# Kernel optimization log

Hardware: AMD Instinct MI355X
Metric: run time of the kernel (lower is better)

## Reference

```python
import jax, jax.numpy as jnp
import numpy as np

EMB = 256
HEADS = 8
D_HEAD = EMB // HEADS


def apply_rope(x):
    # x: [B, H, T, D] (interleaved-pair RoPE, matching the torch source)
    T, D = x.shape[-2], x.shape[-1]
    freqs = 10000.0 ** (-jnp.arange(0, D, 2, dtype=jnp.float32) / D)  # [D/2]
    angles = jnp.arange(T, dtype=jnp.float32)[:, None] * freqs[None, :]  # [T, D/2]
    sin = jnp.repeat(jnp.sin(angles), 2, axis=1)  # [T, D]
    cos = jnp.repeat(jnp.cos(angles), 2, axis=1)  # [T, D]
    x1 = x[..., 0::2]
    x2 = x[..., 1::2]
    rotated = jnp.stack((-x2, x1), axis=-1).reshape(x.shape)  # interleave (-x2, x1)
    return x * cos + rotated * sin


def setup_inputs() -> dict:
    key = jax.random.key(0)
    k1, k2, k3, k4, k5 = jax.random.split(key, 5)
    B, T = 8, 2048
    x = jax.random.normal(k1, (B, T, EMB), dtype=jnp.float32)
    s = 1.0 / np.sqrt(EMB)
    # Linear weights stored as [in, out] (torch weight.T), y = x @ W + b
    Wqkv = jax.random.uniform(k2, (EMB, 3 * EMB), minval=-s, maxval=s, dtype=jnp.float32)
    bqkv = jax.random.uniform(k3, (3 * EMB,), minval=-s, maxval=s, dtype=jnp.float32)
    Wout = jax.random.uniform(k4, (EMB, EMB), minval=-s, maxval=s, dtype=jnp.float32)
    bout = jax.random.uniform(k5, (EMB,), minval=-s, maxval=s, dtype=jnp.float32)
    return {"x": x, "Wqkv": Wqkv, "bqkv": bqkv, "Wout": Wout, "bout": bout}


def reference(x, Wqkv, bqkv, Wout, bout):
    B, T, E = x.shape
    H, Dh = HEADS, D_HEAD
    qkv = x @ Wqkv + bqkv  # [B, T, 3E]
    qkv = qkv.reshape(B, T, 3, H, Dh).transpose(2, 0, 3, 1, 4)  # [3, B, H, T, Dh]
    q, k, v = qkv[0], qkv[1], qkv[2]
    q = apply_rope(q)
    k = apply_rope(k)
    scores = jnp.einsum('bhtd,bhsd->bhts', q, k) / np.sqrt(Dh)  # [B, H, T, T]
    causal = jnp.triu(jnp.ones((T, T), dtype=bool), k=1)
    scores = jnp.where(causal, -jnp.inf, scores)
    attn = jax.nn.softmax(scores, axis=-1)
    out = jnp.einsum('bhts,bhsd->bthd', attn, v).reshape(B, T, E)
    return out @ Wout + bout
```

## Files before the change

### kernel.cpp

```cpp
#include <hip/hip_runtime.h>
#include <hip/hip_bf16.h>
#include <math.h>

typedef __hip_bfloat16 bf16;
using s8v = __attribute__((ext_vector_type(8))) short;
using f4v = __attribute__((ext_vector_type(4))) float;

__device__ __forceinline__ float bfb2f(unsigned short u) {
    return __uint_as_float(((unsigned int)u) << 16);
}
__device__ __forceinline__ unsigned short f2bfb(float f) {
    unsigned int u = __float_as_uint(f);
    unsigned int r = (u + 0x7fffu + ((u >> 16) & 1u)) >> 16;
    return (unsigned short)r;
}
__device__ __forceinline__ unsigned int packbf2(float a, float b) {
    return __builtin_amdgcn_perm(__float_as_uint(b) + 0x8000u,
                                 __float_as_uint(a) + 0x8000u,
                                 0x07060302u);
}

__device__ __forceinline__ void gload_lds16(const void* g, void* l) {
    __builtin_amdgcn_global_load_lds(
        (const __attribute__((address_space(1))) unsigned int*)g,
        (__attribute__((address_space(3))) unsigned int*)l, 16, 0, 0);
}

__device__ __forceinline__ int sniff_fp32(const void* p, int tid, int* s_flag)
{
    if (tid == 0) *s_flag = 0;
    __syncthreads();
    const uint4* u = (const uint4*)p;
    int local = 0;
    #pragma unroll
    for (int i = 0; i < 4; i++) {
        const uint4 v = u[i * 256 + tid];
        if ((v.x & 0x7F80u) == 0x7F80u) local = 1;
        if ((v.y & 0x7F80u) == 0x7F80u) local = 1;
        if ((v.z & 0x7F80u) == 0x7F80u) local = 1;
        if ((v.w & 0x7F80u) == 0x7F80u) local = 1;
    }
    if (local) atomicOr(s_flag, 1);
    __syncthreads();
    return *s_flag;
}

__global__ __launch_bounds__(256)
void k_prep(const void* __restrict__ x, const void* __restrict__ Wqkv,
            const void* __restrict__ bqkv, const void* __restrict__ Wout,
            const void* __restrict__ bout,
            bf16* __restrict__ wqkvT, bf16* __restrict__ woutT,
            float* __restrict__ bq_f, float* __restrict__ bo_f,
            bf16* __restrict__ xb)
{
    __shared__ int sf;
    const int bid = blockIdx.x;
    const int tid = threadIdx.x;
    if (bid < 768) {
        const int f = sniff_fp32(Wqkv, tid, &sf);
        unsigned short v = f ? f2bfb(((const float*)Wqkv)[(size_t)tid * 768 + bid])
                             : ((const unsigned short*)Wqkv)[(size_t)tid * 768 + bid];
        ((unsigned short*)wqkvT)[(size_t)bid * 256 + tid] = v;
        if (bid < 12) {
            const int i = bid * 256 + tid;
            bq_f[i] = f ? ((const float*)bqkv)[i]
                        : bfb2f(((const unsigned short*)bqkv)[i]);
        }
    } else if (bid < 1024) {
        const int n = bid - 768;
        const int f = sniff_fp32(Wout, tid, &sf);
        unsigned short v = f ? f2bfb(((const float*)Wout)[(size_t)tid * 256 + n])
                             : ((const unsigned short*)Wout)[(size_t)tid * 256 + n];
        ((unsigned short*)woutT)[(size_t)n * 256 + tid] = v;
        if (n == 0)
            bo_f[tid] = f ? ((const float*)bout)[tid]
                          : bfb2f(((const unsigned short*)bout)[tid]);
    } else {
        const int f = sniff_fp32(x, tid, &sf);
        if (f) {
            const size_t cb = (size_t)(bid - 1024) * 4096;
            #pragma unroll
            for (int i = 0; i < 4; i++) {
                const size_t e = cb + (size_t)i * 1024 + tid * 4;
                const float4 v = *(const float4*)((const float*)x + e);
                ushort4 o4;
                o4.x = f2bfb(v.x);
                o4.y = f2bfb(v.y);
                o4.z = f2bfb(v.z);
                o4.w = f2bfb(v.w);
                *(ushort4*)((unsigned short*)xb + e) = o4;
            }
        } else {
            const size_t base = (size_t)(bid - 1024) * 4096 + (size_t)tid * 16;
            const uint4* xu = (const uint4*)((const unsigned short*)x + base);
            uint4* dp = (uint4*)((unsigned short*)xb + base);
            dp[0] = xu[0];
            dp[1] = xu[1];
        }
    }
}

__global__ __launch_bounds__(256)
void k_qkv_rope(const bf16* __restrict__ xb, const bf16* __restrict__ wqkvT,
                const float* __restrict__ bq_f,
                bf16* __restrict__ q_ws, bf16* __restrict__ k_ws,
                bf16* __restrict__ vT_ws)
{
    __shared__ __align__(16) unsigned short Bls[4][8][512];
    __shared__ __align__(16) unsigned short Tls[4][1536];

    const int tid = threadIdx.x;
    const int bx = blockIdx.x;
    const int by = blockIdx.y;
    const int n0 = bx * 64;

    const int w    = tid >> 6;
    const int lane = tid & 63;
    const int col  = lane & 15;
    const int quad = lane >> 4;
    const int which = n0 >> 8;
    const int b     = (by * 128) >> 11;
    unsigned short* Tw = Tls[w];

    #pragma unroll
    for (int kk = 0; kk < 8; kk++)
        gload_lds16((const unsigned short*)wqkvT +
                        (size_t)(n0 + w * 16 + col) * 256 + kk * 32 + quad * 8,
                    &Bls[w][kk][0]);
    __syncthreads();

    for (int mi = 0; mi < 2; mi++) {
        const int T0 = by * 128 + mi * 64 + w * 16;

        f4v acc[4] = {{0.f,0.f,0.f,0.f}, {0.f,0.f,0.f,0.f},
                      {0.f,0.f,0.f,0.f}, {0.f,0.f,0.f,0.f}};

        #pragma unroll
        for (int kk = 0; kk < 8; kk++) {
            const s8v av = *(const s8v*)((const unsigned short*)xb +
                           (size_t)(T0 + col) * 256 + kk * 32 + quad * 8);
            #pragma unroll
            for (int c = 0; c < 4; c++) {
                const s8v bv = *(const s8v*)&Bls[c][kk][lane * 8];
                acc[c] = __builtin_amdgcn_mfma_f32_16x16x32_bf16(av, bv, acc[c], 0, 0, 0);
            }
        }

        const int t_base = ((by * 128) & 2047) + mi * 64 + w * 16;

        if (which == 2) {
            #pragma unroll
            for (int c = 0; c < 4; c++) {
                const int nl = c * 16 + col;
                const float bias = bq_f[n0 + nl];
                #pragma unroll
                for (int r = 0; r < 4; r++)
                    Tw[nl * 24 + quad * 4 + r] = f2bfb(acc[c][r] + bias);
            }
            const int ng = n0 + lane;
            const int h = (ng & 255) >> 5;
            const int d = ng & 31;
            const s8v t0 = *(const s8v*)&Tw[lane * 24];
            const s8v t1 = *(const s8v*)&Tw[lane * 24 + 8];
            unsigned short* dp = (unsigned short*)vT_ws +
                ((size_t)(b * 8 + h) * 32 + d) * 2048 + t_base;
            *(s8v*)dp = t0;
            *(s8v*)(dp + 8) = t1;
        } else {
            #pragma unroll
            for (int c = 0; c < 4; c++) {
                const int nl = c * 16 + col;
                const int d = (n0 + nl) & 31;
                const float bias = bq_f[n0 + nl];
                const float frev = __expf(-0.28782314f * (float)(d & ~1))
                                 * 0.15915494309189535f;
                #pragma unroll
                for (int r = 0; r < 4; r++) {
                    const float v = acc[c][r] + bias;
                    const float vp = __shfl_xor(v, 1);
                    const int t = t_base + quad * 4 + r;
                    float rev = (float)t * frev;
                    rev -= floorf(rev);
                    const float ang = rev * 6.283185307179586f;
                    const float sn = __sinf(ang);
                    const float cs = __cosf(ang);
                    float o = (d & 1) ? (v * cs + vp * sn)
                                      : (v * cs - vp * sn);
                    if (which == 0) o *= 0.17677669529663687f;
                    Tw[(quad * 4 + r) * 80 + nl] = f2bfb(o);
                }
            }
            const int row = lane >> 2;
            const int ch  = lane & 3;
            const int ng  = n0 + ch * 16;
            const int h   = (ng & 255) >> 5;
            const int d   = ng & 31;
            const int t   = t_base + row;
            const s8v t0 = *(const s8v*)&Tw[row * 80 + ch * 16];
            const s8v t1 = *(const s8v*)&Tw[row * 80 + ch * 16 + 8];
            unsigned short* dp = (unsigned short*)(which ? k_ws : q_ws) +
                ((size_t)(b * 8 + h) * 2048 + t) * 32 + d;
            *(s8v*)dp = t0;
            *(s8v*)(dp + 8) = t1;
        }
    }
}

__global__ __launch_bounds__(256, 4)
void k_attn(const bf16* __restrict__ q_ws, const bf16* __restrict__ k_ws,
            const bf16* __restrict__ vT_ws, bf16* __restrict__ ctx)
{
    __shared__ __align__(16) unsigned short KVls[2][8][512];
    __shared__ __align__(16) unsigned short Pls[4][16 * 72];

    const int tid  = threadIdx.x;
    const int w    = tid >> 6;
    const int lane = tid & 63;
    const int col  = lane & 15;
    const int quad = lane >> 4;

    const int idx = blockIdx.x;
    const int g   = idx >> 3;
    const int bhh = g >> 4;
    const int bx  = (g + bhh) & 15;
    const int bh  = (bhh << 3) | (idx & 7);
    const int mbA = bx;
    const int mbB = 31 - bx;
    const int T0a = mbA * 64 + w * 16;
    const int T0b = mbB * 64 + w * 16;

    const bf16* qb = q_ws  + (size_t)bh * 65536;
    const bf16* kb = k_ws  + (size_t)bh * 65536;
    const bf16* vb = vT_ws + (size_t)bh * 65536;

    const bf16* kg = kb + (size_t)(w * 16 + col) * 32 + quad * 8;
    const bf16* vg = vb + (size_t)(col + (w & 1) * 16) * 2048
                        + (w >> 1) * 32 + quad * 8;

    const s8v qaA = *(const s8v*)(qb + (size_t)(T0a + col) * 32 + quad * 8);
    const s8v qaB = *(const s8v*)(qb + (size_t)(T0b + col) * 32 + quad * 8);

    f4v oA0 = {0.f,0.f,0.f,0.f}, oA1 = {0.f,0.f,0.f,0.f};
    f4v oB0 = {0.f,0.f,0.f,0.f}, oB1 = {0.f,0.f,0.f,0.f};
    float lpA[4] = {0.f,0.f,0.f,0.f};
    float lpB[4] = {0.f,0.f,0.f,0.f};

    unsigned short* Pw = Pls[w];

    gload_lds16(kg, &KVls[0][w][0]);
    gload_lds16(vg, &KVls[0][4 + w][0]);
    __syncthreads();

    int cur = 0;
    for (int kblk = 0; kblk <= mbB; kblk++) {
        const int s0 = kblk * 64;
        const bool actA = (kblk <= mbA);

        if (kblk < mbB) {
            gload_lds16(kg + (size_t)(kblk + 1) * 2048, &KVls[cur ^ 1][w][0]);
            gload_lds16(vg + (kblk + 1) * 64,           &KVls[cur ^ 1][4 + w][0]);
        }

        const s8v kf0 = *(const s8v*)&KVls[cur][0][lane * 8];
        const s8v kf1 = *(const s8v*)&KVls[cur][1][lane * 8];
        const s8v kf2 = *(const s8v*)&KVls[cur][2][lane * 8];
        const s8v kf3 = *(const s8v*)&KVls[cur][3][lane * 8];
        const s8v v00 = *(const s8v*)&KVls[cur][4][lane * 8];
        const s8v v10 = *(const s8v*)&KVls[cur][5][lane * 8];
        const s8v v01 = *(const s8v*)&KVls[cur][6][lane * 8];
        const s8v v11 = *(const s8v*)&KVls[cur][7][lane * 8];

        const f4v z = {0.f, 0.f, 0.f, 0.f};
        f4v sB[4], sA[4];
        sB[0] = __builtin_amdgcn_mfma_f32_16x16x32_bf16(kf0, qaB, z, 0, 0, 0);
        sB[1] = __builtin_amdgcn_mfma_f32_16x16x32_bf16(kf1, qaB, z, 0, 0, 0);
        sB[2] = __builtin_amdgcn_mfma_f32_16x16x32_bf16(kf2, qaB, z, 0, 0, 0);
        sB[3] = __builtin_amdgcn_mfma_f32_16x16x32_bf16(kf3, qaB, z, 0, 0, 0);
        if (actA) {
            sA[0] = __builtin_amdgcn_mfma_f32_16x16x32_bf16(kf0, qaA, z, 0, 0, 0);
            sA[1] = __builtin_amdgcn_mfma_f32_16x16x32_bf16(kf1, qaA, z, 0, 0, 0);
            sA[2] = __builtin_amdgcn_mfma_f32_16x16x32_bf16(kf2, qaA, z, 0, 0, 0);
            sA[3] = __builtin_amdgcn_mfma_f32_16x16x32_bf16(kf3, qaA, z, 0, 0, 0);
        }

        if (kblk == mbB) {
            #pragma unroll
            for (int c = 0; c < 4; c++) {
                const int sbase = s0 + c * 16 + quad * 4;
                #pragma unroll
                for (int r = 0; r < 4; r++)
                    if (sbase + r > T0b + col) sB[c][r] = -INFINITY;
            }
        }
        if (actA && kblk == mbA) {
            #pragma unroll
            for (int c = 0; c < 4; c++) {
                const int sbase = s0 + c * 16 + quad * 4;
                #pragma unroll
                for (int r = 0; r < 4; r++)
                    if (sbase + r > T0a + col) sA[c][r] = -INFINITY;
            }
        }

        #pragma unroll
        for (int c = 0; c < 4; c++) {
            const float p0 = __expf(sB[c][0]);
            const float p1 = __expf(sB[c][1]);
            const float p2 = __expf(sB[c][2]);
            const float p3 = __expf(sB[c][3]);
            lpB[0] += p0; lpB[1] += p1; lpB[2] += p2; lpB[3] += p3;
            uint2 ww;
            ww.x = packbf2(p0, p1);
            ww.y = packbf2(p2, p3);
            *(uint2*)(Pw + col * 72 + c * 16 + quad * 4) = ww;
        }
        {
            const s8v pb0 = *(const s8v*)&Pw[col * 72 + quad * 8];
            const s8v pb1 = *(const s8v*)&Pw[col * 72 + 32 + quad * 8];
            oB0 = __builtin_amdgcn_mfma_f32_16x16x32_bf16(pb0, v00, oB0, 0, 0, 0);
            oB1 = __builtin_amdgcn_mfma_f32_16x16x32_bf16(pb0, v10, oB1, 0, 0, 0);
            oB0 = __builtin_amdgcn_mfma_f32_16x16x32_bf16(pb1, v01, oB0, 0, 0, 0);
            oB1 = __builtin_amdgcn_mfma_f32_16x16x32_bf16(pb1, v11, oB1, 0, 0, 0);
        }

        if (actA) {
            #pragma unroll
            for (int c = 0; c < 4; c++) {
                const float p0 = __expf(sA[c][0]);
                const float p1 = __expf(sA[c][1]);
                const float p2 = __expf(sA[c][2]);
                const float p3 = __expf(sA[c][3]);
                lpA[0] += p0; lpA[1] += p1; lpA[2] += p2; lpA[3] += p3;
                uint2 ww;
                ww.x = packbf2(p0, p1);
                ww.y = packbf2(p2, p3);
                *(uint2*)(Pw + col * 72 + c * 16 + quad * 4) = ww;
            }
            const s8v pa0 = *(const s8v*)&Pw[col * 72 + quad * 8];
            const s8v pa1 = *(const s8v*)&Pw[col * 72 + 32 + quad * 8];
            oA0 = __builtin_amdgcn_mfma_f32_16x16x32_bf16(pa0, v00, oA0, 0, 0, 0);
            oA1 = __builtin_amdgcn_mfma_f32_16x16x32_bf16(pa0, v10, oA1, 0, 0, 0);
            oA0 = __builtin_amdgcn_mfma_f32_16x16x32_bf16(pa1, v01, oA0, 0, 0, 0);
            oA1 = __builtin_amdgcn_mfma_f32_16x16x32_bf16(pa1, v11, oA1, 0, 0, 0);
        }

        __syncthreads();
        cur ^= 1;
    }

    float rsA = lpA[0] + lpA[1] + lpA[2] + lpA[3];
    rsA += __shfl_xor(rsA, 16);
    rsA += __shfl_xor(rsA, 32);
    float rsB = lpB[0] + lpB[1] + lpB[2] + lpB[3];
    rsB += __shfl_xor(rsB, 16);
    rsB += __shfl_xor(rsB, 32);

    const int b = bh >> 3;
    const int h = bh & 7;
    unsigned short* cp = (unsigned short*)ctx;
    #pragma unroll
    for (int tt = 0; tt < 2; tt++) {
        const int T0 = tt ? T0b : T0a;
        const float rs = tt ? rsB : rsA;
        #pragma unroll
        for (int r = 0; r < 4; r++) {
            const float inv = 1.0f / __shfl(rs, quad * 4 + r);
            const float e0 = (tt ? oB0[r] : oA0[r]) * inv;
            const float e1 = (tt ? oB1[r] : oA1[r]) * inv;
            const int t = T0 + quad * 4 + r;
            unsigned short* dst = cp + (size_t)(b * 2048 + t) * 256 + h * 32;
            dst[col]      = f2bfb(e0);
            dst[col + 16] = f2bfb(e1);
        }
    }
}

__global__ __launch_bounds__(256)
void k_outproj(const bf16* __restrict__ ctx, const bf16* __restrict__ woutT,
               const float* __restrict__ bo_f, float* __restrict__ out)
{
    __shared__ __align__(16) unsigned short Bls[4][8][512];

    const int tid = threadIdx.x;
    const int bx = blockIdx.x;
    const int by = blockIdx.y;
    const int n0 = bx * 64;

    const int w    = tid >> 6;
    const int lane = tid & 63;
    const int col  = lane & 15;
    const int quad = lane >> 4;

    #pragma unroll
    for (int kk = 0; kk < 8; kk++)
        gload_lds16((const unsigned short*)woutT +
                        (size_t)(n0 + w * 16 + col) * 256 + kk * 32 + quad * 8,
                    &Bls[w][kk][0]);
    __syncthreads();

    for (int mi = 0; mi < 2; mi++) {
        const int T0 = by * 128 + mi * 64 + w * 16;

        f4v acc[4] = {{0.f,0.f,0.f,0.f}, {0.f,0.f,0.f,0.f},
                      {0.f,0.f,0.f,0.f}, {0.f,0.f,0.f,0.f}};

        #pragma unroll
        for (int kk = 0; kk < 8; kk++) {
            const s8v av = *(const s8v*)((const unsigned short*)ctx +
                                         (size_t)(T0 + col) * 256 + kk * 32 + quad * 8);
            #pragma unroll
            for (int c = 0; c < 4; c++) {
                const s8v bv = *(const s8v*)&Bls[c][kk][lane * 8];
                acc[c] = __builtin_amdgcn_mfma_f32_16x16x32_bf16(av, bv, acc[c], 0, 0, 0);
            }
        }

        #pragma unroll
        for (int c = 0; c < 4; c++) {
            const int n = n0 + c * 16 + col;
            const float bias = bo_f[n];
            #pragma unroll
            for (int r = 0; r < 4; r++)
                out[(size_t)(T0 + quad * 4 + r) * 256 + n] = acc[c][r] + bias;
        }
    }
}

extern "C" void kernel_launch(void* const* d_in, const int* in_sizes, int n_in,
                              void* d_out, int out_size, void* d_ws, size_t ws_size,
                              hipStream_t stream)
{
    const void* x    = d_in[0];
    const void* Wqkv = d_in[1];
    const void* bqkv = d_in[2];
    const void* Wout = d_in[3];
    const void* bout = d_in[4];
    float* out = (float*)d_out;

    const size_t NQ = (size_t)8 * 8 * 2048 * 32;
    bf16* q_ws   = (bf16*)d_ws;
    bf16* k_ws   = q_ws + NQ;
    bf16* vT_ws  = k_ws + NQ;
    bf16* ctx    = vT_ws + NQ;
    bf16* xb     = ctx;
    bf16* wqkvT  = ctx + NQ;
    bf16* woutT  = wqkvT + (size_t)768 * 256;
    float* bq_f  = (float*)(woutT + (size_t)256 * 256);
    float* bo_f  = bq_f + 3072;

    k_prep    <<<2048,          256, 0, stream>>>(x, Wqkv, bqkv, Wout, bout,
                                                  wqkvT, woutT, bq_f, bo_f, xb);
    k_qkv_rope<<<dim3(12, 128), 256, 0, stream>>>(xb, wqkvT, bq_f,
                                                  q_ws, k_ws, vT_ws);
    k_attn    <<<1024,          256, 0, stream>>>(q_ws, k_ws, vT_ws, ctx);
    k_outproj <<<dim3(4, 128),  256, 0, stream>>>(ctx, woutT, bo_f, out);
}
```

Measured before the change: 158.8 us.

## Replace paired causal query blocks with one query block per attention workgroup

```diff
diff --git a/kernel.cpp b/kernel.cpp
--- a/kernel.cpp
+++ b/kernel.cpp
@@ -220,14 +220,9 @@
     const int quad = lane >> 4;
 
     const int idx = blockIdx.x;
-    const int g   = idx >> 3;
-    const int bhh = g >> 4;
-    const int bx  = (g + bhh) & 15;
-    const int bh  = (bhh << 3) | (idx & 7);
-    const int mbA = bx;
-    const int mbB = 31 - bx;
-    const int T0a = mbA * 64 + w * 16;
-    const int T0b = mbB * 64 + w * 16;
+    const int bh  = idx & 63;
+    const int mb  = 31 - (idx >> 6);
+    const int T0  = mb * 64 + w * 16;
 
     const bf16* qb = q_ws  + (size_t)bh * 65536;
     const bf16* kb = k_ws  + (size_t)bh * 65536;
@@ -237,13 +232,10 @@
     const bf16* vg = vb + (size_t)(col + (w & 1) * 16) * 2048
                         + (w >> 1) * 32 + quad * 8;
 
-    const s8v qaA = *(const s8v*)(qb + (size_t)(T0a + col) * 32 + quad * 8);
-    const s8v qaB = *(const s8v*)(qb + (size_t)(T0b + col) * 32 + quad * 8);
-
-    f4v oA0 = {0.f,0.f,0.f,0.f}, oA1 = {0.f,0.f,0.f,0.f};
-    f4v oB0 = {0.f,0.f,0.f,0.f}, oB1 = {0.f,0.f,0.f,0.f};
-    float lpA[4] = {0.f,0.f,0.f,0.f};
-    float lpB[4] = {0.f,0.f,0.f,0.f};
+    const s8v qa = *(const s8v*)(qb + (size_t)(T0 + col) * 32 + quad * 8);
+
+    f4v o0 = {0.f,0.f,0.f,0.f}, o1 = {0.f,0.f,0.f,0.f};
+    float lp[4] = {0.f,0.f,0.f,0.f};
 
     unsigned short* Pw = Pls[w];
 
@@ -252,13 +244,12 @@
     __syncthreads();
 
     int cur = 0;
-    for (int kblk = 0; kblk <= mbB; kblk++) {
-        const int s0 = kblk * 64;
-        const bool actA = (kblk <= mbA);
-
-        if (kblk < mbB) {
-            gload_lds16(kg + (size_t)(kblk + 1) * 2048, &KVls[cur ^ 1][w][0]);
-            gload_lds16(vg + (kblk + 1) * 64,           &KVls[cur ^ 1][4 + w][0]);
+    for (int kt = 0; kt <= mb; kt++) {
+        const int s0 = kt * 64;
+
+        if (kt < mb) {
+            gload_lds16(kg + (size_t)(kt + 1) * 2048, &KVls[cur ^ 1][w][0]);
+            gload_lds16(vg + (kt + 1) * 64,           &KVls[cur ^ 1][4 + w][0]);
         }
 
         const s8v kf0 = *(const s8v*)&KVls[cur][0][lane * 8];
@@ -271,107 +262,64 @@
         const s8v v11 = *(const s8v*)&KVls[cur][7][lane * 8];
 
         const f4v z = {0.f, 0.f, 0.f, 0.f};
-        f4v sB[4], sA[4];
-        sB[0] = __builtin_amdgcn_mfma_f32_16x16x32_bf16(kf0, qaB, z, 0, 0, 0);
-        sB[1] = __builtin_amdgcn_mfma_f32_16x16x32_bf16(kf1, qaB, z, 0, 0, 0);
-        sB[2] = __builtin_amdgcn_mfma_f32_16x16x32_bf16(kf2, qaB, z, 0, 0, 0);
-        sB[3] = __builtin_amdgcn_mfma_f32_16x16x32_bf16(kf3, qaB, z, 0, 0, 0);
-        if (actA) {
-            sA[0] = __builtin_amdgcn_mfma_f32_16x16x32_bf16(kf0, qaA, z, 0, 0, 0);
-            sA[1] = __builtin_amdgcn_mfma_f32_16x16x32_bf16(kf1, qaA, z, 0, 0, 0);
-            sA[2] = __builtin_amdgcn_mfma_f32_16x16x32_bf16(kf2, qaA, z, 0, 0, 0);
-            sA[3] = __builtin_amdgcn_mfma_f32_16x16x32_bf16(kf3, qaA, z, 0, 0, 0);
-        }
-
-        if (kblk == mbB) {
+        f4v s[4];
+        s[0] = __builtin_amdgcn_mfma_f32_16x16x32_bf16(kf0, qa, z, 0, 0, 0);
+        s[1] = __builtin_amdgcn_mfma_f32_16x16x32_bf16(kf1, qa, z, 0, 0, 0);
+        s[2] = __builtin_amdgcn_mfma_f32_16x16x32_bf16(kf2, qa, z, 0, 0, 0);
+        s[3] = __builtin_amdgcn_mfma_f32_16x16x32_bf16(kf3, qa, z, 0, 0, 0);
+
+        if (kt == mb) {
             #pragma unroll
             for (int c = 0; c < 4; c++) {
                 const int sbase = s0 + c * 16 + quad * 4;
                 #pragma unroll
                 for (int r = 0; r < 4; r++)
-                    if (sbase + r > T0b + col) sB[c][r] = -INFINITY;
-            }
-        }
-        if (actA && kblk == mbA) {
-            #pragma unroll
-            for (int c = 0; c < 4; c++) {
-                const int sbase = s0 + c * 16 + quad * 4;
-                #pragma unroll
-                for (int r = 0; r < 4; r++)
-                    if (sbase + r > T0a + col) sA[c][r] = -INFINITY;
+                    if (sbase + r > T0 + col) s[c][r] = -INFINITY;
             }
         }
 
         #pragma unroll
         for (int c = 0; c < 4; c++) {
-            const float p0 = __expf(sB[c][0]);
-            const float p1 = __expf(sB[c][1]);
-            const float p2 = __expf(sB[c][2]);
-            const float p3 = __expf(sB[c][3]);
-            lpB[0] += p0; lpB[1] += p1; lpB[2] += p2; lpB[3] += p3;
+            const float p0 = __expf(s[c][0]);
+            const float p1 = __expf(s[c][1]);
+            const float p2 = __expf(s[c][2]);
+            const float p3 = __expf(s[c][3]);
+            lp[0] += p0; lp[1] += p1; lp[2] += p2; lp[3] += p3;
             uint2 ww;
             ww.x = packbf2(p0, p1);
             ww.y = packbf2(p2, p3);
             *(uint2*)(Pw + col * 72 + c * 16 + quad * 4) = ww;
         }
+
         {
             const s8v pb0 = *(const s8v*)&Pw[col * 72 + quad * 8];
             const s8v pb1 = *(const s8v*)&Pw[col * 72 + 32 + quad * 8];
-            oB0 = __builtin_amdgcn_mfma_f32_16x16x32_bf16(pb0, v00, oB0, 0, 0, 0);
-            oB1 = __builtin_amdgcn_mfma_f32_16x16x32_bf16(pb0, v10, oB1, 0, 0, 0);
-            oB0 = __builtin_amdgcn_mfma_f32_16x16x32_bf16(pb1, v01, oB0, 0, 0, 0);
-            oB1 = __builtin_amdgcn_mfma_f32_16x16x32_bf16(pb1, v11, oB1, 0, 0, 0);
-        }
-
-        if (actA) {
-            #pragma unroll
-            for (int c = 0; c < 4; c++) {
-                const float p0 = __expf(sA[c][0]);
-                const float p1 = __expf(sA[c][1]);
-                const float p2 = __expf(sA[c][2]);
-                const float p3 = __expf(sA[c][3]);
-                lpA[0] += p0; lpA[1] += p1; lpA[2] += p2; lpA[3] += p3;
-                uint2 ww;
-                ww.x = packbf2(p0, p1);
-                ww.y = packbf2(p2, p3);
-                *(uint2*)(Pw + col * 72 + c * 16 + quad * 4) = ww;
-            }
-            const s8v pa0 = *(const s8v*)&Pw[col * 72 + quad * 8];
-            const s8v pa1 = *(const s8v*)&Pw[col * 72 + 32 + quad * 8];
-            oA0 = __builtin_amdgcn_mfma_f32_16x16x32_bf16(pa0, v00, oA0, 0, 0, 0);
-            oA1 = __builtin_amdgcn_mfma_f32_16x16x32_bf16(pa0, v10, oA1, 0, 0, 0);
-            oA0 = __builtin_amdgcn_mfma_f32_16x16x32_bf16(pa1, v01, oA0, 0, 0, 0);
-            oA1 = __builtin_amdgcn_mfma_f32_16x16x32_bf16(pa1, v11, oA1, 0, 0, 0);
+            o0 = __builtin_amdgcn_mfma_f32_16x16x32_bf16(pb0, v00, o0, 0, 0, 0);
+            o1 = __builtin_amdgcn_mfma_f32_16x16x32_bf16(pb0, v10, o1, 0, 0, 0);
+            o0 = __builtin_amdgcn_mfma_f32_16x16x32_bf16(pb1, v01, o0, 0, 0, 0);
+            o1 = __builtin_amdgcn_mfma_f32_16x16x32_bf16(pb1, v11, o1, 0, 0, 0);
         }
 
         __syncthreads();
         cur ^= 1;
     }
 
-    float rsA = lpA[0] + lpA[1] + lpA[2] + lpA[3];
-    rsA += __shfl_xor(rsA, 16);
-    rsA += __shfl_xor(rsA, 32);
-    float rsB = lpB[0] + lpB[1] + lpB[2] + lpB[3];
-    rsB += __shfl_xor(rsB, 16);
-    rsB += __shfl_xor(rsB, 32);
+    float rs = lp[0] + lp[1] + lp[2] + lp[3];
+    rs += __shfl_xor(rs, 16);
+    rs += __shfl_xor(rs, 32);
 
     const int b = bh >> 3;
     const int h = bh & 7;
     unsigned short* cp = (unsigned short*)ctx;
     #pragma unroll
-    for (int tt = 0; tt < 2; tt++) {
-        const int T0 = tt ? T0b : T0a;
-        const float rs = tt ? rsB : rsA;
-        #pragma unroll
-        for (int r = 0; r < 4; r++) {
-            const float inv = 1.0f / __shfl(rs, quad * 4 + r);
-            const float e0 = (tt ? oB0[r] : oA0[r]) * inv;
-            const float e1 = (tt ? oB1[r] : oA1[r]) * inv;
-            const int t = T0 + quad * 4 + r;
-            unsigned short* dst = cp + (size_t)(b * 2048 + t) * 256 + h * 32;
-            dst[col]      = f2bfb(e0);
-            dst[col + 16] = f2bfb(e1);
-        }
+    for (int r = 0; r < 4; r++) {
+        const float inv = 1.0f / __shfl(rs, quad * 4 + r);
+        const float e0 = o0[r] * inv;
+        const float e1 = o1[r] * inv;
+        const int t = T0 + quad * 4 + r;
+        unsigned short* dst = cp + (size_t)(b * 2048 + t) * 256 + h * 32;
+        dst[col]      = f2bfb(e0);
+        dst[col + 16] = f2bfb(e1);
     }
 }
 
@@ -452,6 +400,6 @@
                                                   wqkvT, woutT, bq_f, bo_f, xb);
     k_qkv_rope<<<dim3(12, 128), 256, 0, stream>>>(xb, wqkvT, bq_f,
                                                   q_ws, k_ws, vT_ws);
-    k_attn    <<<1024,          256, 0, stream>>>(q_ws, k_ws, vT_ws, ctx);
+    k_attn    <<<2048,          256, 0, stream>>>(q_ws, k_ws, vT_ws, ctx);
     k_outproj <<<dim3(4, 128),  256, 0, stream>>>(ctx, woutT, bo_f, out);
 }
```

New measurement: 152.9 us. 3.7% less time.
